# Optimization experiments

Hardware: AMD Instinct MI355X
Metric: run time of the kernel (lower is better)

The kernel has to match this reference:

```python
import jax, jax.numpy as jnp
import numpy as np

N = 20000      # nodes
E = 320000     # edges (avg degree 16)
D = 256        # in_dim == embed_dim
L = 4          # num_layers
G = 128        # number of graphs in the batch
OUT = 64       # out_dim


def setup_inputs() -> dict:
    key = jax.random.key(0)
    ks = jax.random.split(key, 10)
    s = 1.0 / np.sqrt(D)
    x = jax.random.normal(ks[0], (N, D), jnp.float32)
    edge_src = jax.random.randint(ks[1], (E,), 0, N, jnp.int32)
    edge_dst = jax.random.randint(ks[2], (E,), 0, N, jnp.int32)
    batch_ids = jnp.sort(jax.random.randint(ks[3], (N,), 0, G, jnp.int32))
    W1 = jax.random.uniform(ks[4], (L, D, D), jnp.float32, -s, s)
    b1 = jax.random.uniform(ks[5], (L, D), jnp.float32, -s, s)
    W2 = jax.random.uniform(ks[6], (L, D, D), jnp.float32, -s, s)
    b2 = jax.random.uniform(ks[7], (L, D), jnp.float32, -s, s)
    Wout = jax.random.uniform(ks[8], (D, OUT), jnp.float32, -s, s)
    bout = jax.random.uniform(ks[9], (OUT,), jnp.float32, -s, s)
    return {"x": x, "edge_src": edge_src, "edge_dst": edge_dst,
            "batch_ids": batch_ids, "W1": W1, "b1": b1, "W2": W2,
            "b2": b2, "Wout": Wout, "bout": bout}


def reference(x, edge_src, edge_dst, batch_ids, W1, b1, W2, b2, Wout, bout):
    n = x.shape[0]
    h = x
    num_layers = W1.shape[0]
    for i in range(num_layers):
        # GINConv: (1+eps)*x + sum-aggregate of neighbor messages (eps=0)
        agg = jax.ops.segment_sum(h[edge_src], edge_dst, num_segments=n)
        z = h + agg
        # GINConv MLP: Linear -> ReLU -> Linear (plain last)
        z = jnp.maximum(z @ W1[i] + b1[i], 0.0) @ W2[i] + b2[i]
        # BasicGNN inter-layer activation (skipped after last layer, jk=None)
        h = jnp.maximum(z, 0.0) if i < num_layers - 1 else z
    # global_add_pool over graph segment ids
    pooled = jax.ops.segment_sum(h, batch_ids, num_segments=G)  # [G, D]
    out = pooled @ Wout + bout  # [G, OUT]
    return (out, pooled)
```

## Files before the change

### kernel.cpp

```cpp
#include <hip/hip_runtime.h>

#define DIM 256
#define DOUT 64
#define PSPLITS 16

typedef short bf16x8 __attribute__((ext_vector_type(8)));
typedef float f32x4 __attribute__((ext_vector_type(4)));
typedef unsigned short u16x8 __attribute__((ext_vector_type(8)));

static __device__ __forceinline__ float b2f(unsigned short u) {
    return __uint_as_float(((unsigned)u) << 16);
}
static __device__ __forceinline__ unsigned short f2bf(float f) {
    unsigned u = __float_as_uint(f);
    unsigned r = (u + 0x7fffu + ((u >> 16) & 1u)) >> 16;
    return (unsigned short)r;
}

__global__ void cvt_f32_bf16(const float4* __restrict__ src, ushort4* __restrict__ dst, int n4) {
    int i = blockIdx.x * blockDim.x + threadIdx.x;
    int stride = gridDim.x * blockDim.x;
    for (; i < n4; i += stride) {
        float4 v = src[i];
        ushort4 o;
        o.x = f2bf(v.x); o.y = f2bf(v.y); o.z = f2bf(v.z); o.w = f2bf(v.w);
        dst[i] = o;
    }
}

__global__ void copy_i32(const int* __restrict__ src, int* __restrict__ dst, int n) {
    int i = blockIdx.x * blockDim.x + threadIdx.x;
    if (i < n) dst[i] = src[i];
}

__global__ void hist_kernel(const int* __restrict__ dst, int* __restrict__ deg, int E) {
    int i = blockIdx.x * blockDim.x + threadIdx.x;
    if (i < E) atomicAdd(&deg[dst[i]], 1);
}

__global__ void scan_kernel(const int* __restrict__ deg, int* __restrict__ row_ptr, int n) {
    __shared__ int sums[256];
    int t = threadIdx.x;
    int chunk = (n + 255) / 256;
    int lo = t * chunk;
    int hi = min(lo + chunk, n);
    int s = 0;
    for (int i = lo; i < hi; ++i) s += deg[i];
    sums[t] = s;
    __syncthreads();
    for (int off = 1; off < 256; off <<= 1) {
        int v = (t >= off) ? sums[t - off] : 0;
        __syncthreads();
        sums[t] += v;
        __syncthreads();
    }
    int excl = (t == 0) ? 0 : sums[t - 1];
    int run = excl;
    for (int i = lo; i < hi; ++i) { row_ptr[i] = run; run += deg[i]; }
    if (t == 255) row_ptr[n] = run;
}

__global__ void scatter_kernel(const int* __restrict__ src, const int* __restrict__ dst,
                               int* __restrict__ cursor, int* __restrict__ perm, int E) {
    int i = blockIdx.x * blockDim.x + threadIdx.x;
    if (i < E) {
        int d = dst[i];
        int p = atomicAdd(&cursor[d], 1);
        perm[p] = src[i];
    }
}

__global__ void transpose_w(const float* __restrict__ W, unsigned short* __restrict__ Wt) {
    __shared__ float tile[32][33];
    int l = blockIdx.z;
    int k0 = blockIdx.x * 32, n0 = blockIdx.y * 32;
    const float* Wl = W + (size_t)l * DIM * DIM;
    unsigned short* Wtl = Wt + (size_t)l * DIM * DIM;
    int tx = threadIdx.x, ty = threadIdx.y;
    for (int i = ty; i < 32; i += 8)
        tile[i][tx] = Wl[(size_t)(k0 + i) * DIM + n0 + tx];
    __syncthreads();
    for (int i = ty; i < 32; i += 8)
        Wtl[(size_t)(n0 + i) * DIM + k0 + tx] = f2bf(tile[tx][i]);
}

__global__ void agg_kernel(const ushort4* __restrict__ h4, const int* __restrict__ row_ptr,
                           const int* __restrict__ perm, ushort4* __restrict__ z4, int n) {
    int wave = threadIdx.x >> 6;
    int lane = threadIdx.x & 63;
    int node = blockIdx.x * 4 + wave;
    if (node >= n) return;
    size_t base = (size_t)node * 64 + lane;
    ushort4 hv = h4[base];
    float ax = b2f(hv.x), ay = b2f(hv.y), az = b2f(hv.z), aw = b2f(hv.w);
    int lo = row_ptr[node], hi = row_ptr[node + 1];
    int e = lo;
    for (; e + 16 <= hi; e += 16) {
        ushort4 v[16];
#pragma unroll
        for (int j = 0; j < 16; ++j) {
            int s = perm[e + j];
            v[j] = h4[(size_t)s * 64 + lane];
        }
#pragma unroll
        for (int j = 0; j < 16; ++j) {
            ax += b2f(v[j].x); ay += b2f(v[j].y);
            az += b2f(v[j].z); aw += b2f(v[j].w);
        }
    }
    for (; e + 4 <= hi; e += 4) {
        ushort4 v[4];
#pragma unroll
        for (int j = 0; j < 4; ++j) {
            int s = perm[e + j];
            v[j] = h4[(size_t)s * 64 + lane];
        }
#pragma unroll
        for (int j = 0; j < 4; ++j) {
            ax += b2f(v[j].x); ay += b2f(v[j].y);
            az += b2f(v[j].z); aw += b2f(v[j].w);
        }
    }
    for (; e < hi; ++e) {
        int s0 = perm[e];
        ushort4 v0 = h4[(size_t)s0 * 64 + lane];
        ax += b2f(v0.x); ay += b2f(v0.y); az += b2f(v0.z); aw += b2f(v0.w);
    }
    ushort4 o;
    o.x = f2bf(ax); o.y = f2bf(ay); o.z = f2bf(az); o.w = f2bf(aw);
    z4[base] = o;
}

template <bool RELU>
__global__ __launch_bounds__(256, 2) void mfma_gemm(const unsigned short* __restrict__ A,
                                                    const unsigned short* __restrict__ Bt,
                                                    const float* __restrict__ bias,
                                                    unsigned short* __restrict__ C, int M) {
    __shared__ unsigned short Bs[128 * 256];
    const int tid = threadIdx.x;
    const int wave = tid >> 6;
    const int lane = tid & 63;
    const int l15 = lane & 15;
    const int g4 = lane >> 4;
    const int half = blockIdx.x & 1;
    const int mslice = blockIdx.x >> 1;
    const int NT = (M + 15) / 16;

    {
        const char* gsrc = (const char*)&Bt[(size_t)half * 128 * 256];
#pragma unroll
        for (int jj = 0; jj < 16; ++jj) {
            int chunk = tid + jj * 256;
            int col = chunk >> 5;
            int kbyte = (chunk & 31) * 16;
            *reinterpret_cast<u16x8*>((char*)Bs + col * 512 + (kbyte ^ ((col & 7) << 4))) =
                *reinterpret_cast<const u16x8*>(gsrc + col * 512 + kbyte);
        }
    }
    __syncthreads();

    bf16x8 b[4][8];
#pragma unroll
    for (int n = 0; n < 4; ++n) {
        const int col = (wave & 1) * 64 + n * 16 + l15;
        const char* cbase = (const char*)Bs + col * 512;
        const int sw = (col & 7) << 4;
#pragma unroll
        for (int k8 = 0; k8 < 8; ++k8) {
            int kbyte = (k8 * 32 + g4 * 8) * 2;
            b[n][k8] = *reinterpret_cast<const bf16x8*>(cbase + (kbyte ^ sw));
        }
    }

    const int ncol0 = half * 128 + (wave & 1) * 64;
    float bv[4];
#pragma unroll
    for (int n = 0; n < 4; ++n) bv[n] = bias[ncol0 + n * 16 + l15];

    const int base = mslice * 2 + (wave >> 1);

    auto loadA = [&](bf16x8 (&a)[8], int t) {
        int r = t * 16 + l15;
        if (r >= M) r = M - 1;
        const unsigned short* arow = &A[(size_t)r * 256];
#pragma unroll
        for (int k8 = 0; k8 < 8; ++k8)
            a[k8] = *reinterpret_cast<const bf16x8*>(arow + k8 * 32 + g4 * 8);
    };

    auto computeStore = [&](bf16x8 (&a)[8], int t) {
        f32x4 acc[4] = {};
#pragma unroll
        for (int k8 = 0; k8 < 8; ++k8)
#pragma unroll
            for (int n = 0; n < 4; ++n)
                acc[n] = __builtin_amdgcn_mfma_f32_16x16x32_bf16(a[k8], b[n][k8], acc[n], 0, 0, 0);
        int r0 = t * 16 + g4 * 4;
#pragma unroll
        for (int n = 0; n < 4; ++n) {
            int col = ncol0 + n * 16 + l15;
#pragma unroll
            for (int r = 0; r < 4; ++r) {
                int row = r0 + r;
                if (row < M) {
                    float v = acc[n][r] + bv[n];
                    if (RELU) v = fmaxf(v, 0.f);
                    C[(size_t)row * 256 + col] = f2bf(v);
                }
            }
        }
    };

    bf16x8 a0[8], a1[8];
    int t = base;
    if (t >= NT) return;
    loadA(a0, t);
#pragma unroll 1
    for (int rep = 0; rep < 2; ++rep) {
        if (t >= NT) break;
        if (t + 512 < NT) loadA(a1, t + 512);
        computeStore(a0, t);
        t += 512;
        if (t >= NT) break;
        if (t + 512 < NT) loadA(a0, t + 512);
        computeStore(a1, t);
        t += 512;
    }
}

__global__ void gstart_kernel(const int* __restrict__ bids, int* __restrict__ gstart,
                              int n, int G) {
    int g = blockIdx.x * blockDim.x + threadIdx.x;
    if (g > G) return;
    if (g == G) { gstart[G] = n; return; }
    int lo = 0, hi = n;
    while (lo < hi) {
        int mid = (lo + hi) >> 1;
        if (bids[mid] < g) lo = mid + 1; else hi = mid;
    }
    gstart[g] = lo;
}

__global__ void pool_kernel(const ushort4* __restrict__ h4, const int* __restrict__ gstart,
                            float* __restrict__ pooled) {
    int g = blockIdx.x;
    int split = blockIdx.y;
    int lane = threadIdx.x;
    int lo = gstart[g], hi = gstart[g + 1];
    int cnt = hi - lo;
    int chunk = (cnt + PSPLITS - 1) / PSPLITS;
    int s0 = lo + split * chunk;
    int s1 = min(s0 + chunk, hi);
    if (s0 >= s1) return;
    float ax = 0.f, ay = 0.f, az = 0.f, aw = 0.f;
    for (int nd = s0; nd < s1; ++nd) {
        ushort4 v = h4[(size_t)nd * 64 + lane];
        ax += b2f(v.x); ay += b2f(v.y); az += b2f(v.z); aw += b2f(v.w);
    }
    float* p = &pooled[(size_t)g * DIM + lane * 4];
    atomicAdd(p + 0, ax);
    atomicAdd(p + 1, ay);
    atomicAdd(p + 2, az);
    atomicAdd(p + 3, aw);
}

__global__ void out_kernel(const float* __restrict__ pooled, const float* __restrict__ Wout,
                           const float* __restrict__ bout, float* __restrict__ out) {
    __shared__ float p[DIM];
    int g = blockIdx.x;
    for (int d = threadIdx.x; d < DIM; d += blockDim.x) p[d] = pooled[(size_t)g * DIM + d];
    __syncthreads();
    int o = threadIdx.x;
    if (o < DOUT) {
        float acc = bout[o];
        for (int d = 0; d < DIM; ++d) acc += p[d] * Wout[(size_t)d * DOUT + o];
        out[(size_t)g * DOUT + o] = acc;
    }
}

extern "C" void kernel_launch(void* const* d_in, const int* in_sizes, int n_in,
                              void* d_out, int out_size, void* d_ws, size_t ws_size,
                              hipStream_t stream) {
    const float* x    = (const float*)d_in[0];
    const int*   esrc = (const int*)d_in[1];
    const int*   edst = (const int*)d_in[2];
    const int*   bids = (const int*)d_in[3];
    const float* W1   = (const float*)d_in[4];
    const float* b1   = (const float*)d_in[5];
    const float* W2   = (const float*)d_in[6];
    const float* b2   = (const float*)d_in[7];
    const float* Wout = (const float*)d_in[8];
    const float* bout = (const float*)d_in[9];

    const int N = in_sizes[3];
    const int E = in_sizes[1];
    const int L = in_sizes[5] / DIM;
    const int G = out_size / (DOUT + DIM);

    char* ws = (char*)d_ws;
    size_t off = 0;
    auto carve = [&](size_t bytes) -> char* {
        char* p = ws + off;
        off = (off + bytes + 255) & ~(size_t)255;
        return p;
    };
    int* row_ptr = (int*)carve((size_t)(N + 1) * sizeof(int));
    int* cursor  = (int*)carve((size_t)N * sizeof(int));
    int* perm    = (int*)carve((size_t)E * sizeof(int));
    int* gstart  = (int*)carve((size_t)(G + 1) * sizeof(int));
    unsigned short* h   = (unsigned short*)carve((size_t)N * DIM * 2);
    unsigned short* z   = (unsigned short*)carve((size_t)N * DIM * 2);
    unsigned short* t   = (unsigned short*)carve((size_t)N * DIM * 2);
    unsigned short* wt1 = (unsigned short*)carve((size_t)L * DIM * DIM * 2);
    unsigned short* wt2 = (unsigned short*)carve((size_t)L * DIM * DIM * 2);
    (void)ws_size;

    cvt_f32_bf16<<<2048, 256, 0, stream>>>((const float4*)x, (ushort4*)h, N * (DIM / 4));

    hipMemsetAsync(cursor, 0, (size_t)N * sizeof(int), stream);
    hist_kernel<<<(E + 255) / 256, 256, 0, stream>>>(edst, cursor, E);
    scan_kernel<<<1, 256, 0, stream>>>(cursor, row_ptr, N);
    copy_i32<<<(N + 255) / 256, 256, 0, stream>>>(row_ptr, cursor, N);
    scatter_kernel<<<(E + 255) / 256, 256, 0, stream>>>(esrc, edst, cursor, perm, E);

    {
        dim3 tgrid(DIM / 32, DIM / 32, L);
        dim3 tblk(32, 8);
        transpose_w<<<tgrid, tblk, 0, stream>>>(W1, wt1);
        transpose_w<<<tgrid, tblk, 0, stream>>>(W2, wt2);
    }

    for (int l = 0; l < L; ++l) {
        agg_kernel<<<(N + 3) / 4, 256, 0, stream>>>((const ushort4*)h, row_ptr, perm,
                                                    (ushort4*)z, N);
        mfma_gemm<true><<<512, 256, 0, stream>>>(
            z, wt1 + (size_t)l * DIM * DIM, b1 + (size_t)l * DIM, t, N);
        if (l < L - 1)
            mfma_gemm<true><<<512, 256, 0, stream>>>(
                t, wt2 + (size_t)l * DIM * DIM, b2 + (size_t)l * DIM, h, N);
        else
            mfma_gemm<false><<<512, 256, 0, stream>>>(
                t, wt2 + (size_t)l * DIM * DIM, b2 + (size_t)l * DIM, h, N);
    }

    float* outp   = (float*)d_out;
    float* pooled = outp + (size_t)G * DOUT;
    hipMemsetAsync(pooled, 0, (size_t)G * DIM * sizeof(float), stream);
    gstart_kernel<<<1, 256, 0, stream>>>(bids, gstart, N, G);
    {
        dim3 pgrid(G, PSPLITS);
        pool_kernel<<<pgrid, 64, 0, stream>>>((const ushort4*)h, gstart, pooled);
    }
    out_kernel<<<G, 64, 0, stream>>>(pooled, Wout, bout, outp);
}
```

Before: 286.6 us.

## Fuse neighbor aggregation into first MLP GEMM via LDS-staged tiles

```diff
diff --git a/kernel.cpp b/kernel.cpp
--- a/kernel.cpp
+++ b/kernel.cpp
@@ -84,51 +84,118 @@
         Wtl[(size_t)(n0 + i) * DIM + k0 + tx] = f2bf(tile[tx][i]);
 }
 
-__global__ void agg_kernel(const ushort4* __restrict__ h4, const int* __restrict__ row_ptr,
-                           const int* __restrict__ perm, ushort4* __restrict__ z4, int n) {
-    int wave = threadIdx.x >> 6;
-    int lane = threadIdx.x & 63;
-    int node = blockIdx.x * 4 + wave;
-    if (node >= n) return;
-    size_t base = (size_t)node * 64 + lane;
-    ushort4 hv = h4[base];
-    float ax = b2f(hv.x), ay = b2f(hv.y), az = b2f(hv.z), aw = b2f(hv.w);
-    int lo = row_ptr[node], hi = row_ptr[node + 1];
-    int e = lo;
-    for (; e + 16 <= hi; e += 16) {
-        ushort4 v[16];
-#pragma unroll
-        for (int j = 0; j < 16; ++j) {
-            int s = perm[e + j];
-            v[j] = h4[(size_t)s * 64 + lane];
+__global__ __launch_bounds__(512, 2) void fused_agg_gemm1(
+        const unsigned short* __restrict__ H, const int* __restrict__ row_ptr,
+        const int* __restrict__ perm, const unsigned short* __restrict__ Wt1,
+        const float* __restrict__ b1, unsigned short* __restrict__ T, int M) {
+    __shared__ unsigned char lds[147456];
+    char* Ws = (char*)lds;
+    char* Zl = (char*)lds + 131072;
+
+    const int tid = threadIdx.x;
+    const int wave = tid >> 6;
+    const int lane = tid & 63;
+    const int l15 = lane & 15;
+    const int g4 = lane >> 4;
+    const int NTP = (M + 31) / 32;
+
+#pragma unroll
+    for (int jj = 0; jj < 16; ++jj) {
+        int chunk = tid + jj * 512;
+        int col = chunk >> 5;
+        int kbyte = (chunk & 31) * 16;
+        *reinterpret_cast<u16x8*>(Ws + col * 512 + (kbyte ^ ((col & 7) << 4))) =
+            *reinterpret_cast<const u16x8*>((const char*)Wt1 + col * 512 + kbyte);
+    }
+    __syncthreads();
+
+    const int cg = wave & 3;
+    const int mt = wave >> 2;
+    bf16x8 b[4][8];
+#pragma unroll
+    for (int n = 0; n < 4; ++n) {
+        const int col = cg * 64 + n * 16 + l15;
+        const char* cbase = Ws + col * 512;
+        const int sw = (col & 7) << 4;
+#pragma unroll
+        for (int k8 = 0; k8 < 8; ++k8)
+            b[n][k8] = *reinterpret_cast<const bf16x8*>(cbase + ((k8 * 64 + g4 * 16) ^ sw));
+    }
+    float bv[4];
+#pragma unroll
+    for (int n = 0; n < 4; ++n) bv[n] = b1[cg * 64 + n * 16 + l15];
+
+    const int row16 = tid >> 4;
+    const int sl = tid & 15;
+    const int zsw = (row16 & 7) << 4;
+
+    for (int p = blockIdx.x; p < NTP; p += gridDim.x) {
+        {
+            int grow = p * 32 + row16;
+            int row = min(grow, M - 1);
+            const u16x8* hrow = (const u16x8*)(H + (size_t)row * 256);
+            u16x8 own0 = hrow[sl], own1 = hrow[sl + 16];
+            float a0[8], a1[8];
+#pragma unroll
+            for (int j = 0; j < 8; ++j) { a0[j] = b2f(own0[j]); a1[j] = b2f(own1[j]); }
+            int lo = row_ptr[row], hi = row_ptr[row + 1];
+            int e = lo;
+            for (; e + 4 <= hi; e += 4) {
+                u16x8 v0[4], v1[4];
+#pragma unroll
+                for (int j = 0; j < 4; ++j) {
+                    const u16x8* hr = (const u16x8*)(H + (size_t)perm[e + j] * 256);
+                    v0[j] = hr[sl]; v1[j] = hr[sl + 16];
+                }
+#pragma unroll
+                for (int j = 0; j < 4; ++j)
+#pragma unroll
+                    for (int q = 0; q < 8; ++q) { a0[q] += b2f(v0[j][q]); a1[q] += b2f(v1[j][q]); }
+            }
+            for (; e < hi; ++e) {
+                const u16x8* hr = (const u16x8*)(H + (size_t)perm[e] * 256);
+                u16x8 v0 = hr[sl], v1 = hr[sl + 16];
+#pragma unroll
+                for (int q = 0; q < 8; ++q) { a0[q] += b2f(v0[q]); a1[q] += b2f(v1[q]); }
+            }
+            u16x8 o0, o1;
+#pragma unroll
+            for (int j = 0; j < 8; ++j) { o0[j] = f2bf(a0[j]); o1[j] = f2bf(a1[j]); }
+            char* zb = Zl + row16 * 512;
+            *reinterpret_cast<u16x8*>(zb + ((sl * 16) ^ zsw)) = o0;
+            *reinterpret_cast<u16x8*>(zb + (((sl + 16) * 16) ^ zsw)) = o1;
         }
-#pragma unroll
-        for (int j = 0; j < 16; ++j) {
-            ax += b2f(v[j].x); ay += b2f(v[j].y);
-            az += b2f(v[j].z); aw += b2f(v[j].w);
+        __syncthreads();
+
+        {
+            const int rl = mt * 16 + l15;
+            const int rsw = (rl & 7) << 4;
+            bf16x8 a[8];
+#pragma unroll
+            for (int k8 = 0; k8 < 8; ++k8)
+                a[k8] = *reinterpret_cast<const bf16x8*>(
+                    Zl + rl * 512 + ((k8 * 64 + g4 * 16) ^ rsw));
+            f32x4 acc[4] = {};
+#pragma unroll
+            for (int k8 = 0; k8 < 8; ++k8)
+#pragma unroll
+                for (int n = 0; n < 4; ++n)
+                    acc[n] = __builtin_amdgcn_mfma_f32_16x16x32_bf16(a[k8], b[n][k8],
+                                                                     acc[n], 0, 0, 0);
+            int r0 = p * 32 + mt * 16 + g4 * 4;
+#pragma unroll
+            for (int n = 0; n < 4; ++n) {
+                int col = cg * 64 + n * 16 + l15;
+#pragma unroll
+                for (int r = 0; r < 4; ++r) {
+                    int row = r0 + r;
+                    if (row < M)
+                        T[(size_t)row * 256 + col] = f2bf(fmaxf(acc[n][r] + bv[n], 0.f));
+                }
+            }
         }
-    }
-    for (; e + 4 <= hi; e += 4) {
-        ushort4 v[4];
-#pragma unroll
-        for (int j = 0; j < 4; ++j) {
-            int s = perm[e + j];
-            v[j] = h4[(size_t)s * 64 + lane];
-        }
-#pragma unroll
-        for (int j = 0; j < 4; ++j) {
-            ax += b2f(v[j].x); ay += b2f(v[j].y);
-            az += b2f(v[j].z); aw += b2f(v[j].w);
-        }
-    }
-    for (; e < hi; ++e) {
-        int s0 = perm[e];
-        ushort4 v0 = h4[(size_t)s0 * 64 + lane];
-        ax += b2f(v0.x); ay += b2f(v0.y); az += b2f(v0.z); aw += b2f(v0.w);
-    }
-    ushort4 o;
-    o.x = f2bf(ax); o.y = f2bf(ay); o.z = f2bf(az); o.w = f2bf(aw);
-    z4[base] = o;
+        __syncthreads();
+    }
 }
 
 template <bool RELU>
@@ -309,7 +376,6 @@
     int* perm    = (int*)carve((size_t)E * sizeof(int));
     int* gstart  = (int*)carve((size_t)(G + 1) * sizeof(int));
     unsigned short* h   = (unsigned short*)carve((size_t)N * DIM * 2);
-    unsigned short* z   = (unsigned short*)carve((size_t)N * DIM * 2);
     unsigned short* t   = (unsigned short*)carve((size_t)N * DIM * 2);
     unsigned short* wt1 = (unsigned short*)carve((size_t)L * DIM * DIM * 2);
     unsigned short* wt2 = (unsigned short*)carve((size_t)L * DIM * DIM * 2);
@@ -331,10 +397,8 @@
     }
 
     for (int l = 0; l < L; ++l) {
-        agg_kernel<<<(N + 3) / 4, 256, 0, stream>>>((const ushort4*)h, row_ptr, perm,
-                                                    (ushort4*)z, N);
-        mfma_gemm<true><<<512, 256, 0, stream>>>(
-            z, wt1 + (size_t)l * DIM * DIM, b1 + (size_t)l * DIM, t, N);
+        fused_agg_gemm1<<<256, 512, 0, stream>>>(
+            h, row_ptr, perm, wt1 + (size_t)l * DIM * DIM, b1 + (size_t)l * DIM, t, N);
         if (l < L - 1)
             mfma_gemm<true><<<512, 256, 0, stream>>>(
                 t, wt2 + (size_t)l * DIM * DIM, b2 + (size_t)l * DIM, h, N);
```

Result: slower. 301.2 us (+5.1%).

## Pool before last linear layer and fuse scan cursor init

Applied to the files above, without the earlier changes.

```diff
diff --git a/kernel.cpp b/kernel.cpp
--- a/kernel.cpp
+++ b/kernel.cpp
@@ -28,17 +28,12 @@
     }
 }
 
-__global__ void copy_i32(const int* __restrict__ src, int* __restrict__ dst, int n) {
-    int i = blockIdx.x * blockDim.x + threadIdx.x;
-    if (i < n) dst[i] = src[i];
-}
-
 __global__ void hist_kernel(const int* __restrict__ dst, int* __restrict__ deg, int E) {
     int i = blockIdx.x * blockDim.x + threadIdx.x;
     if (i < E) atomicAdd(&deg[dst[i]], 1);
 }
 
-__global__ void scan_kernel(const int* __restrict__ deg, int* __restrict__ row_ptr, int n) {
+__global__ void scan_kernel(int* __restrict__ deg, int* __restrict__ row_ptr, int n) {
     __shared__ int sums[256];
     int t = threadIdx.x;
     int chunk = (n + 255) / 256;
@@ -56,7 +51,12 @@
     }
     int excl = (t == 0) ? 0 : sums[t - 1];
     int run = excl;
-    for (int i = lo; i < hi; ++i) { row_ptr[i] = run; run += deg[i]; }
+    for (int i = lo; i < hi; ++i) {
+        int d = deg[i];
+        row_ptr[i] = run;
+        deg[i] = run;
+        run += d;
+    }
     if (t == 255) row_ptr[n] = run;
 }
 
@@ -264,17 +264,28 @@
     atomicAdd(p + 3, aw);
 }
 
-__global__ void out_kernel(const float* __restrict__ pooled, const float* __restrict__ Wout,
-                           const float* __restrict__ bout, float* __restrict__ out) {
-    __shared__ float p[DIM];
+__global__ void final_kernel(const float* __restrict__ Tp, const int* __restrict__ gstart,
+                             const float* __restrict__ W2, const float* __restrict__ b2,
+                             const float* __restrict__ Wout, const float* __restrict__ bout,
+                             float* __restrict__ out, float* __restrict__ pooled) {
+    __shared__ float tps[DIM];
+    __shared__ float pl[DIM];
     int g = blockIdx.x;
-    for (int d = threadIdx.x; d < DIM; d += blockDim.x) p[d] = pooled[(size_t)g * DIM + d];
-    __syncthreads();
-    int o = threadIdx.x;
-    if (o < DOUT) {
-        float acc = bout[o];
-        for (int d = 0; d < DIM; ++d) acc += p[d] * Wout[(size_t)d * DOUT + o];
-        out[(size_t)g * DOUT + o] = acc;
+    int tidx = threadIdx.x;
+    float cnt = (float)(gstart[g + 1] - gstart[g]);
+    tps[tidx] = Tp[(size_t)g * DIM + tidx];
+    __syncthreads();
+    float acc = cnt * b2[tidx];
+    for (int d = 0; d < DIM; ++d)
+        acc += tps[d] * W2[(size_t)d * DIM + tidx];
+    pooled[(size_t)g * DIM + tidx] = acc;
+    pl[tidx] = acc;
+    __syncthreads();
+    if (tidx < DOUT) {
+        float o = bout[tidx];
+        for (int d = 0; d < DIM; ++d)
+            o += pl[d] * Wout[(size_t)d * DOUT + tidx];
+        out[(size_t)g * DOUT + tidx] = o;
     }
 }
 
@@ -308,6 +319,7 @@
     int* cursor  = (int*)carve((size_t)N * sizeof(int));
     int* perm    = (int*)carve((size_t)E * sizeof(int));
     int* gstart  = (int*)carve((size_t)(G + 1) * sizeof(int));
+    float* Tp    = (float*)carve((size_t)G * DIM * sizeof(float));
     unsigned short* h   = (unsigned short*)carve((size_t)N * DIM * 2);
     unsigned short* z   = (unsigned short*)carve((size_t)N * DIM * 2);
     unsigned short* t   = (unsigned short*)carve((size_t)N * DIM * 2);
@@ -320,7 +332,6 @@
     hipMemsetAsync(cursor, 0, (size_t)N * sizeof(int), stream);
     hist_kernel<<<(E + 255) / 256, 256, 0, stream>>>(edst, cursor, E);
     scan_kernel<<<1, 256, 0, stream>>>(cursor, row_ptr, N);
-    copy_i32<<<(N + 255) / 256, 256, 0, stream>>>(row_ptr, cursor, N);
     scatter_kernel<<<(E + 255) / 256, 256, 0, stream>>>(esrc, edst, cursor, perm, E);
 
     {
@@ -338,18 +349,18 @@
         if (l < L - 1)
             mfma_gemm<true><<<512, 256, 0, stream>>>(
                 t, wt2 + (size_t)l * DIM * DIM, b2 + (size_t)l * DIM, h, N);
-        else
-            mfma_gemm<false><<<512, 256, 0, stream>>>(
-                t, wt2 + (size_t)l * DIM * DIM, b2 + (size_t)l * DIM, h, N);
     }
 
     float* outp   = (float*)d_out;
     float* pooled = outp + (size_t)G * DOUT;
-    hipMemsetAsync(pooled, 0, (size_t)G * DIM * sizeof(float), stream);
+    hipMemsetAsync(Tp, 0, (size_t)G * DIM * sizeof(float), stream);
     gstart_kernel<<<1, 256, 0, stream>>>(bids, gstart, N, G);
     {
         dim3 pgrid(G, PSPLITS);
-        pool_kernel<<<pgrid, 64, 0, stream>>>((const ushort4*)h, gstart, pooled);
-    }
-    out_kernel<<<G, 64, 0, stream>>>(pooled, Wout, bout, outp);
-}
+        pool_kernel<<<pgrid, 64, 0, stream>>>((const ushort4*)t, gstart, Tp);
+    }
+    final_kernel<<<G, 256, 0, stream>>>(Tp, gstart,
+                                        W2 + (size_t)(L - 1) * DIM * DIM,
+                                        b2 + (size_t)(L - 1) * DIM,
+                                        Wout, bout, outp, pooled);
+}
```

New measurement: 292.6 us. 2.1% more time.
